# Kernel tuning notes

Measured on AMD Instinct MI355X. Metric: run time of the kernel, lower is better.

Reference implementation:

```python
import jax, jax.numpy as jnp
import numpy as np

B, S, D = 4, 2048, 512
H, HD, RL = 8, 64, 64   # nheads, head_dim = D//H, rl_dim
TEMPER = 1.0
BETA = 1.0
SLOPE = 0.01  # LeakyReLU negative slope
LN_EPS = 1e-5


def setup_inputs() -> dict:
    key = jax.random.key(0)
    ks = jax.random.split(key, 12)
    scale = 0.02
    return {
        "h":   jax.random.normal(ks[0], (B, S, D), dtype=jnp.float32),
        "rh":  jax.random.normal(ks[1], (B, S, RL), dtype=jnp.float32),
        "Wl":  jax.random.normal(ks[2], (D, D), dtype=jnp.float32) * scale,   # linear_l (in,out)
        "Wr":  jax.random.normal(ks[3], (D, D), dtype=jnp.float32) * scale,   # linear_r
        "al":  jax.random.normal(ks[4], (HD,), dtype=jnp.float32) * scale,    # att_l: Linear(head_dim,1)
        "ar":  jax.random.normal(ks[5], (HD,), dtype=jnp.float32) * scale,    # att_r
        "Wrs": jax.random.normal(ks[6], (RL, RL * H), dtype=jnp.float32) * scale,  # r_source
        "Wrt": jax.random.normal(ks[7], (RL, RL * H), dtype=jnp.float32) * scale,  # r_target
        "Wf":  jax.random.normal(ks[8], (D, D), dtype=jnp.float32) * scale,   # linear_final
        "ln_g": jnp.ones((D,), dtype=jnp.float32),
        "ln_b": jnp.zeros((D,), dtype=jnp.float32),
    }


def _layer_norm(x, g, b):
    mu = jnp.mean(x, axis=-1, keepdims=True)
    var = jnp.mean(jnp.square(x - mu), axis=-1, keepdims=True)
    return (x - mu) * jax.lax.rsqrt(var + LN_EPS) * g + b


def reference(h, rh, Wl, Wr, al, ar, Wrs, Wrt, Wf, ln_g, ln_b):
    leaky = lambda x: jnp.where(x >= 0, x, SLOPE * x)
    # projections -> [B, H, S, HD]
    fl = (h @ Wl).reshape(B, S, H, HD).transpose(0, 2, 1, 3)
    fr = (h @ Wr).reshape(B, S, H, HD).transpose(0, 2, 1, 3)
    # additive attention logits: [B,H,S,1] + [B,H,1,S]
    sl = jnp.einsum('bhsd,d->bhs', leaky(fl), al)
    sr = jnp.einsum('bhsd,d->bhs', leaky(fr), ar)
    score = sl[:, :, :, None] + sr[:, :, None, :]
    # relation-embedding bilinear bias: r_k @ r_q -> [B,H,S,S]
    r_k = (rh @ Wrs).reshape(B, S, H, RL).transpose(0, 2, 1, 3)   # [B,H,S,RL]
    r_q = (rh @ Wrt).reshape(B, S, H, RL).transpose(0, 2, 3, 1)   # [B,H,RL,S]
    score = score + BETA * jnp.einsum('bhsr,bhrt->bhst', r_k, r_q)
    score = jax.nn.softmax(score / TEMPER, axis=-1)
    # context and output projection (dropout = 0 -> identity)
    context = jnp.einsum('bhst,bhtd->bhsd', score, fr)
    h_sa = context.transpose(0, 2, 1, 3).reshape(B, S, H * HD)
    fh = h_sa @ Wf
    return _layer_norm(h + fh, ln_g, ln_b)
```

## Files before the change

kernel.cpp:

```cpp
#include <hip/hip_runtime.h>
#include <math.h>

#define B_ 4
#define S_ 2048
#define D_ 512
#define H_ 8
#define HD_ 64
#define RL_ 64
#define LN_EPS 1e-5f
#define SLOPE 0.01f
#define LOG2E 1.4426950408889634f

typedef __attribute__((ext_vector_type(8))) __bf16 bf16x8;
typedef __attribute__((ext_vector_type(4))) float f32x4;

__device__ __forceinline__ float leaky(float x) { return x >= 0.f ? x : SLOPE * x; }

__device__ __forceinline__ ushort f2bf(float f) {
    union { float f; unsigned u; } v; v.f = f;
    unsigned r = v.u + 0x7fffu + ((v.u >> 16) & 1u);
    return (ushort)(r >> 16);
}
__device__ __forceinline__ unsigned fbits(float f) {
    union { float f; unsigned u; } v; v.f = f; return v.u;
}

__device__ __forceinline__ void g2lds16(const void* g, void* l) {
    __builtin_amdgcn_global_load_lds(
        (const __attribute__((address_space(1))) void*)(uintptr_t)g,
        (__attribute__((address_space(3))) void*)(uintptr_t)l, 16, 0, 0);
}

__global__ __launch_bounds__(256) void prep(
    const float* __restrict__ h, const float* __restrict__ rh,
    const float* __restrict__ Wr, const float* __restrict__ Wf,
    const float* __restrict__ Wrs, const float* __restrict__ Wrt,
    ushort* __restrict__ hb, ushort* __restrict__ rhb,
    ushort* __restrict__ WrT, ushort* __restrict__ WfT,
    ushort* __restrict__ WrsT, ushort* __restrict__ WrtT)
{
    const int bx = blockIdx.x, tid = threadIdx.x;
    if (bx < 4608) {
        const float* in = (bx < 4096) ? h : rh;
        ushort* o = (bx < 4096) ? hb : rhb;
        const int i = (bx < 4096 ? bx : bx - 4096) * 256 + tid;
        const float4 v = ((const float4*)in)[i];
        ushort4 u; u.x = f2bf(v.x); u.y = f2bf(v.y); u.z = f2bf(v.z); u.w = f2bf(v.w);
        ((ushort4*)o)[i] = u;
        return;
    }
    __shared__ float TS[64][65];
    int t = bx - 4608;
    const float* in; ushort* out; int K, tk, tn;
    if (t < 64)       { in = Wr;  out = WrT;  K = 512; tk = t & 7; tn = t >> 3; }
    else if (t < 128) { in = Wf;  out = WfT;  K = 512; t -= 64; tk = t & 7; tn = t >> 3; }
    else if (t < 136) { in = Wrs; out = WrsT; K = 64;  tk = 0; tn = t - 128; }
    else              { in = Wrt; out = WrtT; K = 64;  tk = 0; tn = t - 136; }
    const int k0 = tk * 64, n0 = tn * 64;
    const int r = tid >> 4, c4 = (tid & 15) * 4;
    #pragma unroll
    for (int p = 0; p < 4; ++p) {
        const int row = r + 16 * p;
        const float4 v = *(const float4*)(in + (size_t)(k0 + row) * 512 + n0 + c4);
        TS[row][c4] = v.x; TS[row][c4 + 1] = v.y;
        TS[row][c4 + 2] = v.z; TS[row][c4 + 3] = v.w;
    }
    __syncthreads();
    #pragma unroll
    for (int p = 0; p < 4; ++p) {
        const int nn = r + 16 * p;
        ushort4 o;
        o.x = f2bf(TS[c4 + 0][nn]); o.y = f2bf(TS[c4 + 1][nn]);
        o.z = f2bf(TS[c4 + 2][nn]); o.w = f2bf(TS[c4 + 3][nn]);
        *(ushort4*)(out + (size_t)(n0 + nn) * K + k0 + c4) = o;
    }
}

__global__ __launch_bounds__(256) void proj(
    const ushort* __restrict__ hb, const ushort* __restrict__ rhb,
    const ushort* __restrict__ WrT, const ushort* __restrict__ WrsT,
    const ushort* __restrict__ WrtT,
    ushort* __restrict__ frT, ushort* __restrict__ rkw, ushort* __restrict__ rqw,
    float* __restrict__ sred, const float* __restrict__ ar)
{
    __shared__ ushort As[2][64 * 32];
    __shared__ ushort Bs[2][128 * 32];

    const int tid = threadIdx.x;
    const int lane = tid & 63, w = tid >> 6;
    const int ln = lane & 15, quad = lane >> 4;
    const int wm = w >> 1, wn = w & 1;
    const int m0 = blockIdx.x * 64, n0 = blockIdx.y * 128;
    const int z = blockIdx.z;

    const ushort* A; const ushort* wt; ushort* co; float scl; int K;
    if (z == 0)      { A = hb;  wt = WrT;  co = frT; scl = LOG2E; K = 512; }
    else if (z == 1) { A = rhb; wt = WrsT; co = rkw; scl = LOG2E; K = 64; }
    else             { A = rhb; wt = WrtT; co = rqw; scl = 1.0f;  K = 64; }

    const int srA = tid >> 2;
    const int lchA = ((lane & 3) - (srA >> 1)) & 3;
    const ushort* AgB = A + (size_t)(m0 + srA) * K + lchA * 8;
    const int srB = w * 32 + (lane >> 2);
    const int lchB = ((lane & 3) - (srB >> 1)) & 3;
    const ushort* BgB0 = wt + (size_t)(n0 + srB) * K + lchB * 8;
    const ushort* BgB1 = BgB0 + (size_t)16 * K;
    const int aoff = tid * 8;
    const int boff = srB * 32 + (lane & 3) * 8;
    const int pc = (quad + (ln >> 1)) & 3;

    g2lds16(AgB, &As[0][aoff]);
    g2lds16(BgB0, &Bs[0][boff]);
    g2lds16(BgB1, &Bs[0][boff + 512]);

    f32x4 acc[2][4] = {};
    int buf = 0;
    for (int k0 = 0; k0 < K; k0 += 32) {
        __syncthreads();
        if (k0 + 32 < K) {
            g2lds16(AgB + k0 + 32, &As[buf ^ 1][aoff]);
            g2lds16(BgB0 + k0 + 32, &Bs[buf ^ 1][boff]);
            g2lds16(BgB1 + k0 + 32, &Bs[buf ^ 1][boff + 512]);
        }
        bf16x8 af[2], bfr[4];
        #pragma unroll
        for (int mi = 0; mi < 2; ++mi)
            af[mi] = *(const bf16x8*)&As[buf][(wm * 32 + mi * 16 + ln) * 32 + pc * 8];
        #pragma unroll
        for (int ni = 0; ni < 4; ++ni)
            bfr[ni] = *(const bf16x8*)&Bs[buf][(wn * 64 + ni * 16 + ln) * 32 + pc * 8];
        #pragma unroll
        for (int mi = 0; mi < 2; ++mi)
            #pragma unroll
            for (int ni = 0; ni < 4; ++ni)
                acc[mi][ni] = __builtin_amdgcn_mfma_f32_16x16x32_bf16(
                    af[mi], bfr[ni], acc[mi][ni], 0, 0, 0);
        buf ^= 1;
    }

    const int head = blockIdx.y * 2 + wn;
    const int b = m0 >> 11;
    const size_t bh = (size_t)b * H_ + head;
    if (z == 0) {
        #pragma unroll
        for (int mi = 0; mi < 2; ++mi) {
            const int s = (m0 & (S_ - 1)) + wm * 32 + mi * 16 + quad * 4;
            #pragma unroll
            for (int ni = 0; ni < 4; ++ni) {
                const int d = ni * 16 + ln;
                ushort4 o;
                o.x = f2bf(acc[mi][ni][0]); o.y = f2bf(acc[mi][ni][1]);
                o.z = f2bf(acc[mi][ni][2]); o.w = f2bf(acc[mi][ni][3]);
                *(ushort4*)(co + (bh * 64 + d) * S_ + s) = o;
            }
        }
        float a4[4];
        #pragma unroll
        for (int ni = 0; ni < 4; ++ni) a4[ni] = ar[ni * 16 + ln];
        #pragma unroll
        for (int mi = 0; mi < 2; ++mi) {
            const int s = (m0 & (S_ - 1)) + wm * 32 + mi * 16 + quad * 4;
            #pragma unroll
            for (int r = 0; r < 4; ++r) {
                float v = 0.f;
                #pragma unroll
                for (int ni = 0; ni < 4; ++ni)
                    v += leaky(acc[mi][ni][r]) * a4[ni];
                #pragma unroll
                for (int off = 8; off; off >>= 1) v += __shfl_xor(v, off, 16);
                if (ln == 0) sred[bh * S_ + s + r] = v * scl;
            }
        }
    } else {
        #pragma unroll
        for (int mi = 0; mi < 2; ++mi) {
            const int s = (m0 & (S_ - 1)) + wm * 32 + mi * 16 + quad * 4;
            #pragma unroll
            for (int ni = 0; ni < 4; ++ni) {
                const int d = ni * 16 + ln;
                #pragma unroll
                for (int r = 0; r < 4; ++r)
                    co[(bh * S_ + s + r) * 64 + d] = f2bf(acc[mi][ni][r] * scl);
            }
        }
    }
}

__global__ __launch_bounds__(256, 2) void attn_mfma(
    const ushort* __restrict__ frT, const ushort* __restrict__ rk,
    const ushort* __restrict__ rq, const float* __restrict__ sr,
    ushort* __restrict__ hsa)
{
    __shared__ ushort RQ[2][64][64];
    __shared__ ushort FT[2][64][64];
    __shared__ ushort PS[8][16][64];

    const int tid = threadIdx.x;
    const int w = tid >> 6;
    const int lane = tid & 63;
    const int ln = lane & 15;
    const int quad = lane >> 4;
    const int b = blockIdx.z, h = blockIdx.y, q0 = blockIdx.x * 128;
    const size_t bh = (size_t)b * H_ + h;

    bf16x8 a[2][2];
    #pragma unroll
    for (int qs = 0; qs < 2; ++qs) {
        const ushort* p = rk + ((bh * S_ + q0 + 32 * w + 16 * qs + ln) << 6);
        a[qs][0] = *(const bf16x8*)(p + quad * 8);
        a[qs][1] = *(const bf16x8*)(p + 32 + quad * 8);
    }

    const ushort* rq_g = rq + (bh * S_ << 6);
    const ushort* ft_g = frT + (size_t)bh * 64 * S_;
    const float* srp = sr + bh * S_;

    const int rl = lane >> 3;
    const int pg = lane & 7;
    const int row_b = w * 16 + rl;
    const int sgF = (pg - rl) & 7;
    const int sgR0 = (pg - 4 * w - (rl >> 2)) & 7;
    const int sgR1 = (pg - 4 * w - 2 - (rl >> 2)) & 7;

    #define STAGE(BUF, t0)                                                    \
        {                                                                     \
            g2lds16(rq_g + ((size_t)((t0) + row_b) << 6) + sgR0 * 8,          \
                    &RQ[BUF][row_b][pg * 8]);                                 \
            g2lds16(rq_g + ((size_t)((t0) + row_b + 8) << 6) + sgR1 * 8,      \
                    &RQ[BUF][row_b + 8][pg * 8]);                             \
            g2lds16(ft_g + (size_t)row_b * S_ + (t0) + sgF * 8,               \
                    &FT[BUF][row_b][pg * 8]);                                 \
            g2lds16(ft_g + (size_t)(row_b + 8) * S_ + (t0) + sgF * 8,         \
                    &FT[BUF][row_b + 8][pg * 8]);                             \
        }

    const ushort* rqrA = &RQ[0][0][0] + 4 * ln * 64 + ((quad + ln) & 7) * 8;
    const ushort* rqrB = &RQ[0][0][0] + 4 * ln * 64 + ((quad + 4 + ln) & 7) * 8;
    const ushort* ftrA = &FT[0][0][0] + ln * 64 + ((quad + ln) & 7) * 8;
    const ushort* ftrB = &FT[0][0][0] + ln * 64 + ((quad + 4 + ln) & 7) * 8;
    ushort* sb[2];
    sb[0] = &PS[w * 2][0][0]; sb[1] = &PS[w * 2 + 1][0][0];
    int wr_off[4];
    #pragma unroll
    for (int r = 0; r < 4; ++r) {
        const int prow = quad * 4 + r;
        wr_off[r] = prow * 64 + (((ln >> 1) + prow) & 7) * 8 + (ln & 1) * 4;
    }
    const int rd0 = ln * 64 + ((quad + ln) & 7) * 8;
    const int rd1 = ln * 64 + ((quad + 4 + ln) & 7) * 8;

    STAGE(0, 0)
    __syncthreads();

    float lsum[2][4] = {};
    f32x4 ctx[2][4] = {};

    for (int t0 = 0; t0 < S_; t0 += 128) {
        #pragma unroll
        for (int half = 0; half < 2; ++half) {
            const int tc = t0 + 64 * half;
            if (tc + 64 < S_) {
                if (half == 0) STAGE(1, tc + 64)
                else           STAGE(0, tc + 64)
            }
            const float4 srv = *(const float4*)(srp + tc + 4 * ln);

            f32x4 sc[2][4];
            #pragma unroll
            for (int jb = 0; jb < 4; ++jb) {
                const bf16x8 b0 = *(const bf16x8*)(rqrA + half * 4096 + jb * 64);
                const bf16x8 b1 = *(const bf16x8*)(rqrB + half * 4096 + jb * 64);
                #pragma unroll
                for (int qs = 0; qs < 2; ++qs) {
                    f32x4 t = {0.f, 0.f, 0.f, 0.f};
                    t = __builtin_amdgcn_mfma_f32_16x16x32_bf16(a[qs][0], b0, t, 0, 0, 0);
                    t = __builtin_amdgcn_mfma_f32_16x16x32_bf16(a[qs][1], b1, t, 0, 0, 0);
                    sc[qs][jb] = t;
                }
            }

            #pragma unroll
            for (int qs = 0; qs < 2; ++qs)
                #pragma unroll
                for (int r = 0; r < 4; ++r) {
                    const float p0 = __builtin_amdgcn_exp2f(sc[qs][0][r] + srv.x);
                    const float p1 = __builtin_amdgcn_exp2f(sc[qs][1][r] + srv.y);
                    const float p2 = __builtin_amdgcn_exp2f(sc[qs][2][r] + srv.z);
                    const float p3 = __builtin_amdgcn_exp2f(sc[qs][3][r] + srv.w);
                    lsum[qs][r] += (p0 + p1) + (p2 + p3);
                    const unsigned lo = (fbits(p0) >> 16) | (fbits(p1) & 0xffff0000u);
                    const unsigned hi = (fbits(p2) >> 16) | (fbits(p3) & 0xffff0000u);
                    *(uint2*)(sb[qs] + wr_off[r]) = make_uint2(lo, hi);
                }

            const bf16x8 pa00 = *(const bf16x8*)(sb[0] + rd0);
            const bf16x8 pa01 = *(const bf16x8*)(sb[0] + rd1);
            const bf16x8 pa10 = *(const bf16x8*)(sb[1] + rd0);
            const bf16x8 pa11 = *(const bf16x8*)(sb[1] + rd1);
            #pragma unroll
            for (int jb = 0; jb < 4; ++jb) {
                const bf16x8 fb0 = *(const bf16x8*)(ftrA + half * 4096 + jb * 1024);
                const bf16x8 fb1 = *(const bf16x8*)(ftrB + half * 4096 + jb * 1024);
                ctx[0][jb] = __builtin_amdgcn_mfma_f32_16x16x32_bf16(pa00, fb0, ctx[0][jb], 0, 0, 0);
                ctx[0][jb] = __builtin_amdgcn_mfma_f32_16x16x32_bf16(pa01, fb1, ctx[0][jb], 0, 0, 0);
                ctx[1][jb] = __builtin_amdgcn_mfma_f32_16x16x32_bf16(pa10, fb0, ctx[1][jb], 0, 0, 0);
                ctx[1][jb] = __builtin_amdgcn_mfma_f32_16x16x32_bf16(pa11, fb1, ctx[1][jb], 0, 0, 0);
            }

            __syncthreads();
        }
    }

    #pragma unroll
    for (int qs = 0; qs < 2; ++qs)
        #pragma unroll
        for (int r = 0; r < 4; ++r) {
            float l = lsum[qs][r];
            #pragma unroll
            for (int off = 8; off; off >>= 1) l += __shfl_xor(l, off, 16);
            const float inv = 1.f / l;
            const int q = q0 + 32 * w + 16 * qs + quad * 4 + r;
            ushort* orow = hsa + (size_t)(b * S_ + q) * D_ + h * 64;
            #pragma unroll
            for (int jb = 0; jb < 4; ++jb)
                orow[16 * jb + ln] = f2bf(ctx[qs][jb][r] * inv);
        }
}

__global__ __launch_bounds__(256) void gemm_out(
    const ushort* __restrict__ A, const ushort* __restrict__ WT,
    float* __restrict__ C)
{
    __shared__ ushort As[2][64 * 32];
    __shared__ ushort Bs[2][128 * 32];

    const int tid = threadIdx.x;
    const int lane = tid & 63, w = tid >> 6;
    const int ln = lane & 15, quad = lane >> 4;
    const int wm = w >> 1, wn = w & 1;
    const int m0 = blockIdx.x * 64, n0 = blockIdx.y * 128;
    const int K = 512;

    const int srA = tid >> 2;
    const int lchA = ((lane & 3) - (srA >> 1)) & 3;
    const ushort* AgB = A + (size_t)(m0 + srA) * K + lchA * 8;
    const int srB = w * 32 + (lane >> 2);
    const int lchB = ((lane & 3) - (srB >> 1)) & 3;
    const ushort* BgB0 = WT + (size_t)(n0 + srB) * K + lchB * 8;
    const ushort* BgB1 = BgB0 + (size_t)16 * K;
    const int aoff = tid * 8;
    const int boff = srB * 32 + (lane & 3) * 8;
    const int pc = (quad + (ln >> 1)) & 3;

    g2lds16(AgB, &As[0][aoff]);
    g2lds16(BgB0, &Bs[0][boff]);
    g2lds16(BgB1, &Bs[0][boff + 512]);

    f32x4 acc[2][4] = {};
    int buf = 0;
    for (int k0 = 0; k0 < K; k0 += 32) {
        __syncthreads();
        if (k0 + 32 < K) {
            g2lds16(AgB + k0 + 32, &As[buf ^ 1][aoff]);
            g2lds16(BgB0 + k0 + 32, &Bs[buf ^ 1][boff]);
            g2lds16(BgB1 + k0 + 32, &Bs[buf ^ 1][boff + 512]);
        }
        bf16x8 af[2], bfr[4];
        #pragma unroll
        for (int mi = 0; mi < 2; ++mi)
            af[mi] = *(const bf16x8*)&As[buf][(wm * 32 + mi * 16 + ln) * 32 + pc * 8];
        #pragma unroll
        for (int ni = 0; ni < 4; ++ni)
            bfr[ni] = *(const bf16x8*)&Bs[buf][(wn * 64 + ni * 16 + ln) * 32 + pc * 8];
        #pragma unroll
        for (int mi = 0; mi < 2; ++mi)
            #pragma unroll
            for (int ni = 0; ni < 4; ++ni)
                acc[mi][ni] = __builtin_amdgcn_mfma_f32_16x16x32_bf16(
                    af[mi], bfr[ni], acc[mi][ni], 0, 0, 0);
        buf ^= 1;
    }

    #pragma unroll
    for (int mi = 0; mi < 2; ++mi) {
        const int row = m0 + wm * 32 + mi * 16 + quad * 4;
        #pragma unroll
        for (int ni = 0; ni < 4; ++ni) {
            const int col = n0 + wn * 64 + ni * 16 + ln;
            #pragma unroll
            for (int r = 0; r < 4; ++r)
                C[(size_t)(row + r) * 512 + col] = acc[mi][ni][r];
        }
    }
}

__global__ __launch_bounds__(256) void ln_kernel(
    const float* __restrict__ h, const float* __restrict__ fh,
    const float* __restrict__ g, const float* __restrict__ bb,
    float* __restrict__ out)
{
    const int row = blockIdx.x, tid = threadIdx.x;
    const float* hp = h + (size_t)row * 512;
    const float* fp = fh + (size_t)row * 512;
    const float x0 = hp[tid] + fp[tid];
    const float x1 = hp[tid + 256] + fp[tid + 256];
    __shared__ float red[4];

    float s = x0 + x1;
    #pragma unroll
    for (int off = 32; off; off >>= 1) s += __shfl_xor(s, off, 64);
    if ((tid & 63) == 0) red[tid >> 6] = s;
    __syncthreads();
    const float mu = (red[0] + red[1] + red[2] + red[3]) * (1.f / 512.f);

    const float d0 = x0 - mu, d1 = x1 - mu;
    float v = d0 * d0 + d1 * d1;
    #pragma unroll
    for (int off = 32; off; off >>= 1) v += __shfl_xor(v, off, 64);
    __syncthreads();
    if ((tid & 63) == 0) red[tid >> 6] = v;
    __syncthreads();
    const float var = (red[0] + red[1] + red[2] + red[3]) * (1.f / 512.f);
    const float inv = rsqrtf(var + LN_EPS);

    out[(size_t)row * 512 + tid] = d0 * inv * g[tid] + bb[tid];
    out[(size_t)row * 512 + tid + 256] = d1 * inv * g[tid + 256] + bb[tid + 256];
}

extern "C" void kernel_launch(void* const* d_in, const int* in_sizes, int n_in,
                              void* d_out, int out_size, void* d_ws, size_t ws_size,
                              hipStream_t stream)
{
    const float* h   = (const float*)d_in[0];
    const float* rh  = (const float*)d_in[1];
    const float* Wr  = (const float*)d_in[3];
    const float* ar  = (const float*)d_in[5];
    const float* Wrs = (const float*)d_in[6];
    const float* Wrt = (const float*)d_in[7];
    const float* Wf  = (const float*)d_in[8];
    const float* lng = (const float*)d_in[9];
    const float* lnb = (const float*)d_in[10];
    float* out = (float*)d_out;
    char* wsb  = (char*)d_ws;

    const size_t MB = (size_t)1 << 20;
    ushort* hb   = (ushort*)(wsb);
    ushort* rhb  = (ushort*)(wsb + 8 * MB);
    ushort* WrT  = (ushort*)(wsb + 9 * MB);
    ushort* WfT  = (ushort*)(wsb + 9 * MB + 512 * 1024);
    ushort* WrsT = (ushort*)(wsb + 10 * MB);
    ushort* WrtT = (ushort*)(wsb + 10 * MB + 64 * 1024);
    ushort* frT  = (ushort*)(wsb + 11 * MB);
    ushort* rkw  = (ushort*)(wsb + 19 * MB);
    ushort* rqw  = (ushort*)(wsb + 27 * MB);
    float*  sr   = (float*) (wsb + 35 * MB);
    ushort* hsab = (ushort*)(wsb + 36 * MB);
    float*  fh   = (float*) (wsb + 44 * MB);

    dim3 blk(256);
    prep<<<dim3(4752), blk, 0, stream>>>(h, rh, Wr, Wf, Wrs, Wrt,
                                         hb, rhb, WrT, WfT, WrsT, WrtT);
    proj<<<dim3(128, 4, 3), blk, 0, stream>>>(hb, rhb, WrT, WrsT, WrtT,
                                              frT, rkw, rqw, sr, ar);
    attn_mfma<<<dim3(S_ / 128, H_, B_), blk, 0, stream>>>(frT, rkw, rqw, sr, hsab);
    gemm_out<<<dim3(128, 4), blk, 0, stream>>>(hsab, WfT, fh);
    ln_kernel<<<dim3(B_ * S_), blk, 0, stream>>>(h, fh, lng, lnb, out);
}
```

Measured before the change: 174.1 us.

## Halve attention query tile to 64 rows and remap blocks across XCDs

Measured after the change: 177.9 us. 1.02x slower.

```diff
diff --git a/kernel.cpp b/kernel.cpp
--- a/kernel.cpp
+++ b/kernel.cpp
@@ -186,29 +186,33 @@
     }
 }
 
-__global__ __launch_bounds__(256, 2) void attn_mfma(
+__global__ __launch_bounds__(256, 4) void attn_mfma(
     const ushort* __restrict__ frT, const ushort* __restrict__ rk,
     const ushort* __restrict__ rq, const float* __restrict__ sr,
     ushort* __restrict__ hsa)
 {
     __shared__ ushort RQ[2][64][64];
     __shared__ ushort FT[2][64][64];
-    __shared__ ushort PS[8][16][64];
+    __shared__ ushort PS[4][16][64];
 
     const int tid = threadIdx.x;
     const int w = tid >> 6;
     const int lane = tid & 63;
     const int ln = lane & 15;
     const int quad = lane >> 4;
-    const int b = blockIdx.z, h = blockIdx.y, q0 = blockIdx.x * 128;
+
+    const int flat = blockIdx.x + 32 * (blockIdx.y + 8 * blockIdx.z);
+    const int wid = (flat & 7) * 128 + (flat >> 3);
+    const int q0 = (wid & 31) * 64;
+    const int h = (wid >> 5) & 7;
+    const int b = wid >> 8;
     const size_t bh = (size_t)b * H_ + h;
 
-    bf16x8 a[2][2];
-    #pragma unroll
-    for (int qs = 0; qs < 2; ++qs) {
-        const ushort* p = rk + ((bh * S_ + q0 + 32 * w + 16 * qs + ln) << 6);
-        a[qs][0] = *(const bf16x8*)(p + quad * 8);
-        a[qs][1] = *(const bf16x8*)(p + 32 + quad * 8);
+    bf16x8 a[2];
+    {
+        const ushort* p = rk + ((bh * S_ + q0 + 16 * w + ln) << 6);
+        a[0] = *(const bf16x8*)(p + quad * 8);
+        a[1] = *(const bf16x8*)(p + 32 + quad * 8);
     }
 
     const ushort* rq_g = rq + (bh * S_ << 6);
@@ -238,8 +242,7 @@
     const ushort* rqrB = &RQ[0][0][0] + 4 * ln * 64 + ((quad + 4 + ln) & 7) * 8;
     const ushort* ftrA = &FT[0][0][0] + ln * 64 + ((quad + ln) & 7) * 8;
     const ushort* ftrB = &FT[0][0][0] + ln * 64 + ((quad + 4 + ln) & 7) * 8;
-    ushort* sb[2];
-    sb[0] = &PS[w * 2][0][0]; sb[1] = &PS[w * 2 + 1][0][0];
+    ushort* sb = &PS[w][0][0];
     int wr_off[4];
     #pragma unroll
     for (int r = 0; r < 4; ++r) {
@@ -252,8 +255,8 @@
     STAGE(0, 0)
     __syncthreads();
 
-    float lsum[2][4] = {};
-    f32x4 ctx[2][4] = {};
+    float lsum[4] = {};
+    f32x4 ctx[4] = {};
 
     for (int t0 = 0; t0 < S_; t0 += 128) {
         #pragma unroll
@@ -265,46 +268,37 @@
             }
             const float4 srv = *(const float4*)(srp + tc + 4 * ln);
 
-            f32x4 sc[2][4];
+            f32x4 sc[4];
             #pragma unroll
             for (int jb = 0; jb < 4; ++jb) {
                 const bf16x8 b0 = *(const bf16x8*)(rqrA + half * 4096 + jb * 64);
                 const bf16x8 b1 = *(const bf16x8*)(rqrB + half * 4096 + jb * 64);
-                #pragma unroll
-                for (int qs = 0; qs < 2; ++qs) {
-                    f32x4 t = {0.f, 0.f, 0.f, 0.f};
-                    t = __builtin_amdgcn_mfma_f32_16x16x32_bf16(a[qs][0], b0, t, 0, 0, 0);
-                    t = __builtin_amdgcn_mfma_f32_16x16x32_bf16(a[qs][1], b1, t, 0, 0, 0);
-                    sc[qs][jb] = t;
-                }
-            }
-
-            #pragma unroll
-            for (int qs = 0; qs < 2; ++qs)
-                #pragma unroll
-                for (int r = 0; r < 4; ++r) {
-                    const float p0 = __builtin_amdgcn_exp2f(sc[qs][0][r] + srv.x);
-                    const float p1 = __builtin_amdgcn_exp2f(sc[qs][1][r] + srv.y);
-                    const float p2 = __builtin_amdgcn_exp2f(sc[qs][2][r] + srv.z);
-                    const float p3 = __builtin_amdgcn_exp2f(sc[qs][3][r] + srv.w);
-                    lsum[qs][r] += (p0 + p1) + (p2 + p3);
-                    const unsigned lo = (fbits(p0) >> 16) | (fbits(p1) & 0xffff0000u);
-                    const unsigned hi = (fbits(p2) >> 16) | (fbits(p3) & 0xffff0000u);
-                    *(uint2*)(sb[qs] + wr_off[r]) = make_uint2(lo, hi);
-                }
-
-            const bf16x8 pa00 = *(const bf16x8*)(sb[0] + rd0);
-            const bf16x8 pa01 = *(const bf16x8*)(sb[0] + rd1);
-            const bf16x8 pa10 = *(const bf16x8*)(sb[1] + rd0);
-            const bf16x8 pa11 = *(const bf16x8*)(sb[1] + rd1);
+                f32x4 t = {0.f, 0.f, 0.f, 0.f};
+                t = __builtin_amdgcn_mfma_f32_16x16x32_bf16(a[0], b0, t, 0, 0, 0);
+                t = __builtin_amdgcn_mfma_f32_16x16x32_bf16(a[1], b1, t, 0, 0, 0);
+                sc[jb] = t;
+            }
+
+            #pragma unroll
+            for (int r = 0; r < 4; ++r) {
+                const float p0 = __builtin_amdgcn_exp2f(sc[0][r] + srv.x);
+                const float p1 = __builtin_amdgcn_exp2f(sc[1][r] + srv.y);
+                const float p2 = __builtin_amdgcn_exp2f(sc[2][r] + srv.z);
+                const float p3 = __builtin_amdgcn_exp2f(sc[3][r] + srv.w);
+                lsum[r] += (p0 + p1) + (p2 + p3);
+                const unsigned lo = (fbits(p0) >> 16) | (fbits(p1) & 0xffff0000u);
+                const unsigned hi = (fbits(p2) >> 16) | (fbits(p3) & 0xffff0000u);
+                *(uint2*)(sb + wr_off[r]) = make_uint2(lo, hi);
+            }
+
+            const bf16x8 pa0 = *(const bf16x8*)(sb + rd0);
+            const bf16x8 pa1 = *(const bf16x8*)(sb + rd1);
             #pragma unroll
             for (int jb = 0; jb < 4; ++jb) {
                 const bf16x8 fb0 = *(const bf16x8*)(ftrA + half * 4096 + jb * 1024);
                 const bf16x8 fb1 = *(const bf16x8*)(ftrB + half * 4096 + jb * 1024);
-                ctx[0][jb] = __builtin_amdgcn_mfma_f32_16x16x32_bf16(pa00, fb0, ctx[0][jb], 0, 0, 0);
-                ctx[0][jb] = __builtin_amdgcn_mfma_f32_16x16x32_bf16(pa01, fb1, ctx[0][jb], 0, 0, 0);
-                ctx[1][jb] = __builtin_amdgcn_mfma_f32_16x16x32_bf16(pa10, fb0, ctx[1][jb], 0, 0, 0);
-                ctx[1][jb] = __builtin_amdgcn_mfma_f32_16x16x32_bf16(pa11, fb1, ctx[1][jb], 0, 0, 0);
+                ctx[jb] = __builtin_amdgcn_mfma_f32_16x16x32_bf16(pa0, fb0, ctx[jb], 0, 0, 0);
+                ctx[jb] = __builtin_amdgcn_mfma_f32_16x16x32_bf16(pa1, fb1, ctx[jb], 0, 0, 0);
             }
 
             __syncthreads();
@@ -312,19 +306,17 @@
     }
 
     #pragma unroll
-    for (int qs = 0; qs < 2; ++qs)
-        #pragma unroll
-        for (int r = 0; r < 4; ++r) {
-            float l = lsum[qs][r];
-            #pragma unroll
-            for (int off = 8; off; off >>= 1) l += __shfl_xor(l, off, 16);
-            const float inv = 1.f / l;
-            const int q = q0 + 32 * w + 16 * qs + quad * 4 + r;
-            ushort* orow = hsa + (size_t)(b * S_ + q) * D_ + h * 64;
-            #pragma unroll
-            for (int jb = 0; jb < 4; ++jb)
-                orow[16 * jb + ln] = f2bf(ctx[qs][jb][r] * inv);
-        }
+    for (int r = 0; r < 4; ++r) {
+        float l = lsum[r];
+        #pragma unroll
+        for (int off = 8; off; off >>= 1) l += __shfl_xor(l, off, 16);
+        const float inv = 1.f / l;
+        const int q = q0 + 16 * w + quad * 4 + r;
+        ushort* orow = hsa + (size_t)(b * S_ + q) * D_ + h * 64;
+        #pragma unroll
+        for (int jb = 0; jb < 4; ++jb)
+            orow[16 * jb + ln] = f2bf(ctx[jb][r] * inv);
+    }
 }
 
 __global__ __launch_bounds__(256) void gemm_out(
@@ -462,7 +454,7 @@
                                          hb, rhb, WrT, WfT, WrsT, WrtT);
     proj<<<dim3(128, 4, 3), blk, 0, stream>>>(hb, rhb, WrT, WrsT, WrtT,
                                               frT, rkw, rqw, sr, ar);
-    attn_mfma<<<dim3(S_ / 128, H_, B_), blk, 0, stream>>>(frT, rkw, rqw, sr, hsab);
+    attn_mfma<<<dim3(S_ / 64, H_, B_), blk, 0, stream>>>(frT, rkw, rqw, sr, hsab);
     gemm_out<<<dim3(128, 4), blk, 0, stream>>>(hsab, WfT, fh);
     ln_kernel<<<dim3(B_ * S_), blk, 0, stream>>>(h, fh, lng, lnb, out);
 }
```

## Deepen attention LDS pipeline to four stages with explicit vmcnt waits and block swizzle

Applied to the files above, without the earlier changes.

New measurement: 172.4 us. Within noise of the previous version (-1.0%).

```diff
diff --git a/kernel.cpp b/kernel.cpp
--- a/kernel.cpp
+++ b/kernel.cpp
@@ -186,13 +186,16 @@
     }
 }
 
+#define WAITV(N) asm volatile("s_waitcnt vmcnt(" #N ")" ::: "memory")
+#define BARR()   __builtin_amdgcn_s_barrier()
+
 __global__ __launch_bounds__(256, 2) void attn_mfma(
     const ushort* __restrict__ frT, const ushort* __restrict__ rk,
     const ushort* __restrict__ rq, const float* __restrict__ sr,
     ushort* __restrict__ hsa)
 {
-    __shared__ ushort RQ[2][64][64];
-    __shared__ ushort FT[2][64][64];
+    __shared__ ushort RQ[4][64][64];
+    __shared__ ushort FT[4][64][64];
     __shared__ ushort PS[8][16][64];
 
     const int tid = threadIdx.x;
@@ -200,7 +203,12 @@
     const int lane = tid & 63;
     const int ln = lane & 15;
     const int quad = lane >> 4;
-    const int b = blockIdx.z, h = blockIdx.y, q0 = blockIdx.x * 128;
+
+    const int flat = blockIdx.x + 16 * (blockIdx.y + 8 * blockIdx.z);
+    const int wid = (flat & 7) * 64 + (flat >> 3);
+    const int q0 = (wid & 15) * 128;
+    const int h = (wid >> 4) & 7;
+    const int b = wid >> 7;
     const size_t bh = (size_t)b * H_ + h;
 
     bf16x8 a[2][2];
@@ -249,67 +257,81 @@
     const int rd0 = ln * 64 + ((quad + ln) & 7) * 8;
     const int rd1 = ln * 64 + ((quad + 4 + ln) & 7) * 8;
 
-    STAGE(0, 0)
-    __syncthreads();
-
     float lsum[2][4] = {};
     f32x4 ctx[2][4] = {};
 
-    for (int t0 = 0; t0 < S_; t0 += 128) {
-        #pragma unroll
-        for (int half = 0; half < 2; ++half) {
-            const int tc = t0 + 64 * half;
-            if (tc + 64 < S_) {
-                if (half == 0) STAGE(1, tc + 64)
-                else           STAGE(0, tc + 64)
-            }
-            const float4 srv = *(const float4*)(srp + tc + 4 * ln);
-
-            f32x4 sc[2][4];
-            #pragma unroll
-            for (int jb = 0; jb < 4; ++jb) {
-                const bf16x8 b0 = *(const bf16x8*)(rqrA + half * 4096 + jb * 64);
-                const bf16x8 b1 = *(const bf16x8*)(rqrB + half * 4096 + jb * 64);
-                #pragma unroll
-                for (int qs = 0; qs < 2; ++qs) {
-                    f32x4 t = {0.f, 0.f, 0.f, 0.f};
-                    t = __builtin_amdgcn_mfma_f32_16x16x32_bf16(a[qs][0], b0, t, 0, 0, 0);
-                    t = __builtin_amdgcn_mfma_f32_16x16x32_bf16(a[qs][1], b1, t, 0, 0, 0);
-                    sc[qs][jb] = t;
-                }
-            }
-
-            #pragma unroll
-            for (int qs = 0; qs < 2; ++qs)
-                #pragma unroll
-                for (int r = 0; r < 4; ++r) {
-                    const float p0 = __builtin_amdgcn_exp2f(sc[qs][0][r] + srv.x);
-                    const float p1 = __builtin_amdgcn_exp2f(sc[qs][1][r] + srv.y);
-                    const float p2 = __builtin_amdgcn_exp2f(sc[qs][2][r] + srv.z);
-                    const float p3 = __builtin_amdgcn_exp2f(sc[qs][3][r] + srv.w);
-                    lsum[qs][r] += (p0 + p1) + (p2 + p3);
-                    const unsigned lo = (fbits(p0) >> 16) | (fbits(p1) & 0xffff0000u);
-                    const unsigned hi = (fbits(p2) >> 16) | (fbits(p3) & 0xffff0000u);
-                    *(uint2*)(sb[qs] + wr_off[r]) = make_uint2(lo, hi);
-                }
-
-            const bf16x8 pa00 = *(const bf16x8*)(sb[0] + rd0);
-            const bf16x8 pa01 = *(const bf16x8*)(sb[0] + rd1);
-            const bf16x8 pa10 = *(const bf16x8*)(sb[1] + rd0);
-            const bf16x8 pa11 = *(const bf16x8*)(sb[1] + rd1);
-            #pragma unroll
-            for (int jb = 0; jb < 4; ++jb) {
-                const bf16x8 fb0 = *(const bf16x8*)(ftrA + half * 4096 + jb * 1024);
-                const bf16x8 fb1 = *(const bf16x8*)(ftrB + half * 4096 + jb * 1024);
-                ctx[0][jb] = __builtin_amdgcn_mfma_f32_16x16x32_bf16(pa00, fb0, ctx[0][jb], 0, 0, 0);
-                ctx[0][jb] = __builtin_amdgcn_mfma_f32_16x16x32_bf16(pa01, fb1, ctx[0][jb], 0, 0, 0);
-                ctx[1][jb] = __builtin_amdgcn_mfma_f32_16x16x32_bf16(pa10, fb0, ctx[1][jb], 0, 0, 0);
-                ctx[1][jb] = __builtin_amdgcn_mfma_f32_16x16x32_bf16(pa11, fb1, ctx[1][jb], 0, 0, 0);
-            }
-
-            __syncthreads();
-        }
-    }
+    #define COMPUTE(BI, SV)                                                        \
+        {                                                                          \
+            f32x4 sc[2][4];                                                        \
+            _Pragma("unroll")                                                      \
+            for (int jb = 0; jb < 4; ++jb) {                                       \
+                const bf16x8 b0 = *(const bf16x8*)(rqrA + (BI) * 4096 + jb * 64);  \
+                const bf16x8 b1 = *(const bf16x8*)(rqrB + (BI) * 4096 + jb * 64);  \
+                _Pragma("unroll")                                                  \
+                for (int qs = 0; qs < 2; ++qs) {                                   \
+                    f32x4 tt = {0.f, 0.f, 0.f, 0.f};                               \
+                    tt = __builtin_amdgcn_mfma_f32_16x16x32_bf16(a[qs][0], b0, tt, 0, 0, 0); \
+                    tt = __builtin_amdgcn_mfma_f32_16x16x32_bf16(a[qs][1], b1, tt, 0, 0, 0); \
+                    sc[qs][jb] = tt;                                               \
+                }                                                                  \
+            }                                                                      \
+            _Pragma("unroll")                                                      \
+            for (int qs = 0; qs < 2; ++qs)                                         \
+                _Pragma("unroll")                                                  \
+                for (int r = 0; r < 4; ++r) {                                      \
+                    const float p0 = __builtin_amdgcn_exp2f(sc[qs][0][r] + SV.x);  \
+                    const float p1 = __builtin_amdgcn_exp2f(sc[qs][1][r] + SV.y);  \
+                    const float p2 = __builtin_amdgcn_exp2f(sc[qs][2][r] + SV.z);  \
+                    const float p3 = __builtin_amdgcn_exp2f(sc[qs][3][r] + SV.w);  \
+                    lsum[qs][r] += (p0 + p1) + (p2 + p3);                          \
+                    const unsigned lo = (fbits(p0) >> 16) | (fbits(p1) & 0xffff0000u); \
+                    const unsigned hi = (fbits(p2) >> 16) | (fbits(p3) & 0xffff0000u); \
+                    *(uint2*)(sb[qs] + wr_off[r]) = make_uint2(lo, hi);            \
+                }                                                                  \
+            const bf16x8 pa00 = *(const bf16x8*)(sb[0] + rd0);                     \
+            const bf16x8 pa01 = *(const bf16x8*)(sb[0] + rd1);                     \
+            const bf16x8 pa10 = *(const bf16x8*)(sb[1] + rd0);                     \
+            const bf16x8 pa11 = *(const bf16x8*)(sb[1] + rd1);                     \
+            _Pragma("unroll")                                                      \
+            for (int jb = 0; jb < 4; ++jb) {                                       \
+                const bf16x8 fb0 = *(const bf16x8*)(ftrA + (BI) * 4096 + jb * 1024); \
+                const bf16x8 fb1 = *(const bf16x8*)(ftrB + (BI) * 4096 + jb * 1024); \
+                ctx[0][jb] = __builtin_amdgcn_mfma_f32_16x16x32_bf16(pa00, fb0, ctx[0][jb], 0, 0, 0); \
+                ctx[0][jb] = __builtin_amdgcn_mfma_f32_16x16x32_bf16(pa01, fb1, ctx[0][jb], 0, 0, 0); \
+                ctx[1][jb] = __builtin_amdgcn_mfma_f32_16x16x32_bf16(pa10, fb0, ctx[1][jb], 0, 0, 0); \
+                ctx[1][jb] = __builtin_amdgcn_mfma_f32_16x16x32_bf16(pa11, fb1, ctx[1][jb], 0, 0, 0); \
+            }                                                                      \
+        }
+
+    float4 sv0, sv1, sv2, sv3;
+    STAGE(0, 0)   sv0 = *(const float4*)(srp + 0 + 4 * ln);
+    STAGE(1, 64)  sv1 = *(const float4*)(srp + 64 + 4 * ln);
+
+    for (int it = 0; it < 7; ++it) {
+        const int t0 = it * 256;
+        WAITV(5); BARR();
+        STAGE(2, t0 + 128) sv2 = *(const float4*)(srp + t0 + 128 + 4 * ln);
+        COMPUTE(0, sv0)
+        WAITV(5); BARR();
+        STAGE(3, t0 + 192) sv3 = *(const float4*)(srp + t0 + 192 + 4 * ln);
+        COMPUTE(1, sv1)
+        WAITV(5); BARR();
+        STAGE(0, t0 + 256) sv0 = *(const float4*)(srp + t0 + 256 + 4 * ln);
+        COMPUTE(2, sv2)
+        WAITV(5); BARR();
+        STAGE(1, t0 + 320) sv1 = *(const float4*)(srp + t0 + 320 + 4 * ln);
+        COMPUTE(3, sv3)
+    }
+    WAITV(5); BARR();
+    STAGE(2, 1920) sv2 = *(const float4*)(srp + 1920 + 4 * ln);
+    COMPUTE(0, sv0)
+    WAITV(5); BARR();
+    STAGE(3, 1984) sv3 = *(const float4*)(srp + 1984 + 4 * ln);
+    COMPUTE(1, sv1)
+    WAITV(5); BARR();
+    COMPUTE(2, sv2)
+    WAITV(0); BARR();
+    COMPUTE(3, sv3)
 
     #pragma unroll
     for (int qs = 0; qs < 2; ++qs)
```
